# Optimization experiments

Hardware: AMD Instinct MI355X
Metric: run time of the kernel (lower is better)

## Reference

```python
import jax, jax.numpy as jnp
import numpy as np

D_MODEL = 512

def setup_inputs() -> dict:
    key = jax.random.key(0)
    k1, k2, k3 = jax.random.split(key, 3)
    B, N1, N2 = 16, 2048, 2048
    x1 = jax.random.normal(k1, (B, N1, D_MODEL), dtype=jnp.float32)
    x2 = jax.random.normal(k2, (B, N2, D_MODEL), dtype=jnp.float32)
    node_mask = jnp.ones((B, N1), dtype=jnp.bool_)
    # learned parameter: q_proj weight, stored torch-style [out, in]
    Wq = jax.random.normal(k3, (D_MODEL, D_MODEL), dtype=jnp.float32) * (1.0 / np.sqrt(D_MODEL))
    return {"x1": x1, "x2": x2, "node_mask": node_mask, "Wq": Wq}


def reference(x1, x2, node_mask, Wq):
    # Q = x1 @ Wq^T   (torch Linear with weight [out, in], no bias)
    Q = jnp.einsum('bnd,ed->bne', x1, Wq)            # [B, N1, 512]
    D = x2                                            # [B, N2, 512]
    # similarity matrix L = Q @ D^T
    L = jnp.einsum('bnd,bmd->bnm', Q, D)              # [B, N1, N2]
    # attention over document axis (dim=2)
    A_D = jax.nn.softmax(L, axis=2)                   # [B, N1, N2]
    # C_D = Q^T @ A_D -> transposed to [B, N2, 512]
    C_D = jnp.einsum('bnd,bnm->bmd', Q, A_D)          # [B, N2, 512]
    # attention over query axis (dim=1), then transposed: A_Q [B, N2, N1]
    A_Q = jnp.swapaxes(jax.nn.softmax(L, axis=1), 1, 2)
    # C_Q = D^T @ A_Q -> transposed to [B, N1, 512]
    C_Q = jnp.einsum('bmd,bmn->bnd', D, A_Q)          # [B, N1, 512]
    return (C_Q, C_D, A_D, A_Q)
```

## Files before the change

### kernel.cpp

```cpp
#include <hip/hip_runtime.h>

namespace {

constexpr int Bn = 16;
constexpr int Nn = 2048;
constexpr int Dn = 512;

typedef _Float16 h4 __attribute__((ext_vector_type(4)));
typedef _Float16 h8 __attribute__((ext_vector_type(8)));
typedef float    fx4 __attribute__((ext_vector_type(4)));

__device__ __forceinline__ void gld16(const _Float16* g, _Float16* l) {
  typedef const void __attribute__((address_space(1))) gvoid;
  typedef void __attribute__((address_space(3))) lvoid;
  __builtin_amdgcn_global_load_lds((gvoid*)g, (lvoid*)l, 16, 0, 0);
}

__device__ __forceinline__ void stage_gld(const _Float16* __restrict__ g, int ld,
    int r0, int k0, _Float16* __restrict__ lds, int t)
{
  #pragma unroll
  for (int i = 0; i < 2; ++i) {
    int chunk = i*256 + t;
    gld16(g + (long)(r0 + (chunk >> 2))*ld + k0 + (chunk & 3)*8, lds + chunk*8);
  }
}

__device__ __forceinline__ void stage_gld256(const _Float16* __restrict__ g, int ld,
    int r0, int k0, _Float16* __restrict__ lds, int t)
{
  #pragma unroll
  for (int i = 0; i < 4; ++i) {
    int chunk = i*256 + t;
    gld16(g + (long)(r0 + (chunk >> 2))*ld + k0 + (chunk & 3)*8, lds + chunk*8);
  }
}

__device__ __forceinline__ void load_f32(const float* __restrict__ g, int ld,
    int r0, int k0, int t, fx4* regs)
{
  #pragma unroll
  for (int rd = 0; rd < 4; ++rd)
    regs[rd] = *(const fx4*)(g + (long)(r0 + rd*32 + (t >> 3))*ld + k0 + (t & 7)*4);
}
template<int S>
__device__ __forceinline__ void write_cvt(const fx4* regs, _Float16* __restrict__ lds, int t)
{
  const int c = (t & 7)*4;
  #pragma unroll
  for (int rd = 0; rd < 4; ++rd) {
    int r = rd*32 + (t >> 3);
    h4 o;
    #pragma unroll
    for (int i = 0; i < 4; ++i) o[i] = (_Float16)regs[rd][i];
    *(h4*)(lds + r*S + c) = o;
  }
}

struct RegsA3 { h8 v0, v1; fx4 k00, k01, k10, k11; };
__device__ __forceinline__ void load_A3(const _Float16* __restrict__ g, int ld,
    int r0, int k0, int t, const float* __restrict__ kofs, RegsA3& R)
{
  {
    int chunk = t, r = chunk >> 2, c = (chunk & 3)*8;
    R.v0  = *(const h8*)(g + (long)(r0 + r)*ld + k0 + c);
    R.k00 = *(const fx4*)(kofs + k0 + c);
    R.k01 = *(const fx4*)(kofs + k0 + c + 4);
  }
  {
    int chunk = 256 + t, r = chunk >> 2, c = (chunk & 3)*8;
    R.v1  = *(const h8*)(g + (long)(r0 + r)*ld + k0 + c);
    R.k10 = *(const fx4*)(kofs + k0 + c);
    R.k11 = *(const fx4*)(kofs + k0 + c + 4);
  }
}
template<int S>
__device__ __forceinline__ void write_A3(const RegsA3& R, _Float16* __restrict__ lds, int t)
{
  {
    int chunk = t, r = chunk >> 2, c = (chunk & 3)*8;
    h8 o;
    #pragma unroll
    for (int j = 0; j < 4; ++j) {
      o[j]   = (_Float16)__expf((float)R.v0[j]   - R.k00[j]);
      o[4+j] = (_Float16)__expf((float)R.v0[4+j] - R.k01[j]);
    }
    *(h8*)(lds + r*S + c) = o;
  }
  {
    int chunk = 256 + t, r = chunk >> 2, c = (chunk & 3)*8;
    h8 o;
    #pragma unroll
    for (int j = 0; j < 4; ++j) {
      o[j]   = (_Float16)__expf((float)R.v1[j]   - R.k10[j]);
      o[4+j] = (_Float16)__expf((float)R.v1[4+j] - R.k11[j]);
    }
    *(h8*)(lds + r*S + c) = o;
  }
}

template<int MA, int MB, int EPI, int TY>
__global__ __launch_bounds__(256) void gemm128(
    const void* __restrict__ Ap, long sA,
    const void* __restrict__ Bp, long sB,
    void* __restrict__ Cp, long sC, int ldc,
    void* __restrict__ C2p, long sC2, int ldc2,
    int lda, int ldb, int K,
    const float* __restrict__ kofs,
    float* __restrict__ rowPM, float* __restrict__ rowPS,
    float* __restrict__ colPM, float* __restrict__ colPS)
{
  constexpr int SA = (MA == 0) ? 32 : 40;
  constexpr int SB = (MB == 0) ? 32 : 40;
  constexpr int ASZ = 128*SA, BSZ = 128*SB;
  constexpr int DB = 2*ASZ + 2*BSZ;
  constexpr int SMEM = (EPI >= 1 && DB < 128*136) ? 128*136 : DB;
  __shared__ _Float16 smem[SMEM];

  constexpr int TILES = 16*TY;
  const int bid = blockIdx.x;
  const int xcd = bid & 7, slot = bid >> 3;
  const int b = xcd*2 + slot/TILES;
  const int tile = slot % TILES;
  const int by = tile % TY, bx = tile / TY;
  const int row0 = bx*128, col0 = by*128;

  const int t = threadIdx.x, w = t >> 6, l = t & 63;
  const int wr = w >> 1, wc = w & 1, l15 = l & 15, lg = l >> 4;

  const void* Ab;
  const void* Bb;
  if constexpr (MA == 1) Ab = (const void*)((const float*)Ap + (long)b*sA);
  else                   Ab = (const void*)((const _Float16*)Ap + (long)b*sA);
  if constexpr (MB == 1) Bb = (const void*)((const float*)Bp + (long)b*sB);
  else                   Bb = (const void*)((const _Float16*)Bp + (long)b*sB);

  const float* ko = nullptr;
  if constexpr (MA == 3) ko = kofs + (long)b*Nn;

  fx4 acc[4][4];
  #pragma unroll
  for (int fi = 0; fi < 4; ++fi)
    #pragma unroll
    for (int fj = 0; fj < 4; ++fj)
      acc[fi][fj] = (fx4){0.f, 0.f, 0.f, 0.f};

  const int NT = K/32;
  fx4 regA[4], regB[4];
  RegsA3 rA3;

  if constexpr (MA == 0)      stage_gld((const _Float16*)Ab, lda, row0, 0, smem, t);
  else if constexpr (MA == 1) load_f32((const float*)Ab, lda, row0, 0, t, regA);
  else                        load_A3((const _Float16*)Ab, lda, row0, 0, t, ko, rA3);
  if constexpr (MB == 0)      stage_gld((const _Float16*)Bb, ldb, col0, 0, smem + 2*ASZ, t);
  else                        load_f32((const float*)Bb, ldb, col0, 0, t, regB);
  if constexpr (MA == 1)      write_cvt<SA>(regA, smem, t);
  if constexpr (MA == 3)      write_A3<SA>(rA3, smem, t);
  if constexpr (MB == 1)      write_cvt<SB>(regB, smem + 2*ASZ, t);
  __syncthreads();

  for (int kt = 0; kt < NT; ++kt) {
    const int cur = kt & 1, nxt = cur ^ 1;
    const int k1 = (kt + 1)*32;
    _Float16* cA = smem + cur*ASZ;
    _Float16* cB = smem + 2*ASZ + cur*BSZ;
    _Float16* nA = smem + nxt*ASZ;
    _Float16* nB = smem + 2*ASZ + nxt*BSZ;

    if (kt + 1 < NT) {
      if constexpr (MA == 0)      stage_gld((const _Float16*)Ab, lda, row0, k1, nA, t);
      else if constexpr (MA == 1) load_f32((const float*)Ab, lda, row0, k1, t, regA);
      else                        load_A3((const _Float16*)Ab, lda, row0, k1, t, ko, rA3);
      if constexpr (MB == 0)      stage_gld((const _Float16*)Bb, ldb, col0, k1, nB, t);
      else                        load_f32((const float*)Bb, ldb, col0, k1, t, regB);
    }

    h8 af[4], bf[4];
    #pragma unroll
    for (int fi = 0; fi < 4; ++fi)
      af[fi] = *(const h8*)(cA + (wr*64 + fi*16 + l15)*SA + lg*8);
    #pragma unroll
    for (int fj = 0; fj < 4; ++fj)
      bf[fj] = *(const h8*)(cB + (wc*64 + fj*16 + l15)*SB + lg*8);
    #pragma unroll
    for (int fi = 0; fi < 4; ++fi)
      #pragma unroll
      for (int fj = 0; fj < 4; ++fj)
        acc[fi][fj] = __builtin_amdgcn_mfma_f32_16x16x32_f16(af[fi], bf[fj], acc[fi][fj], 0, 0, 0);

    if (kt + 1 < NT) {
      if constexpr (MA == 1) write_cvt<SA>(regA, nA, t);
      if constexpr (MA == 3) write_A3<SA>(rA3, nA, t);
      if constexpr (MB == 1) write_cvt<SB>(regB, nB, t);
    }
    __syncthreads();
  }

  if constexpr (EPI == 0) {
    float* Cb = (float*)Cp + (long)b*sC;
    #pragma unroll
    for (int fi = 0; fi < 4; ++fi)
      #pragma unroll
      for (int fj = 0; fj < 4; ++fj)
        #pragma unroll
        for (int j = 0; j < 4; ++j)
          Cb[(long)(row0 + wr*64 + fi*16 + lg*4 + j)*ldc + col0 + wc*64 + fj*16 + l15] = acc[fi][fj][j];
  }

  if constexpr (EPI >= 1) {
    if constexpr (EPI == 1) {
      #pragma unroll
      for (int fi = 0; fi < 4; ++fi)
        #pragma unroll
        for (int fj = 0; fj < 4; ++fj)
          #pragma unroll
          for (int j = 0; j < 4; ++j)
            acc[fi][fj][j] = (float)(_Float16)acc[fi][fj][j];
    }

    #pragma unroll
    for (int fi = 0; fi < 4; ++fi) {
      #pragma unroll
      for (int j = 0; j < 4; ++j) {
        int rr = wr*64 + fi*16 + lg*4 + j;
        int key = (rr >> 3) & 7;
        #pragma unroll
        for (int fj = 0; fj < 4; ++fj) {
          int cc = wc*64 + fj*16 + l15;
          smem[rr*136 + ((((cc >> 3) ^ key) << 3) | (cc & 7))] = (_Float16)acc[fi][fj][j];
        }
      }
    }
    __syncthreads();
    _Float16* Cb  = (_Float16*)Cp  + (long)b*sC;
    _Float16* C2b = (_Float16*)C2p + (long)b*sC2;
    #pragma unroll
    for (int rd = 0; rd < 8; ++rd) {
      int r = rd*16 + (t >> 4);
      int g = (t & 15) ^ ((r >> 3) & 7);
      h8 v = *(const h8*)(smem + r*136 + g*8);
      *(h8*)(Cb + (long)(row0 + r)*ldc + col0 + (t & 15)*8) = v;
    }
    {
      const int q = t & 15, keyq = q & 7, n8 = q*8;
      #pragma unroll
      for (int rd = 0; rd < 8; ++rd) {
        int dl = rd*16 + (t >> 4);
        int gbase = ((dl >> 3) ^ keyq) << 3, c7 = dl & 7;
        h8 v;
        #pragma unroll
        for (int i = 0; i < 8; ++i)
          v[i] = smem[(n8 + i)*136 + gbase + c7];
        *(h8*)(C2b + (long)(col0 + dl)*ldc2 + row0 + n8) = v;
      }
    }
  }

  if constexpr (EPI == 1) {
    float rm[4][4], rs[4][4];
    #pragma unroll
    for (int fi = 0; fi < 4; ++fi)
      #pragma unroll
      for (int j = 0; j < 4; ++j)
        rm[fi][j] = fmaxf(fmaxf(acc[fi][0][j], acc[fi][1][j]),
                          fmaxf(acc[fi][2][j], acc[fi][3][j]));
    #pragma unroll
    for (int m = 1; m < 16; m <<= 1)
      #pragma unroll
      for (int fi = 0; fi < 4; ++fi)
        #pragma unroll
        for (int j = 0; j < 4; ++j)
          rm[fi][j] = fmaxf(rm[fi][j], __shfl_xor(rm[fi][j], m, 64));
    #pragma unroll
    for (int fi = 0; fi < 4; ++fi)
      #pragma unroll
      for (int j = 0; j < 4; ++j) {
        float s = 0.f;
        #pragma unroll
        for (int fj = 0; fj < 4; ++fj)
          s += __expf(acc[fi][fj][j] - rm[fi][j]);
        rs[fi][j] = s;
      }
    #pragma unroll
    for (int m = 1; m < 16; m <<= 1)
      #pragma unroll
      for (int fi = 0; fi < 4; ++fi)
        #pragma unroll
        for (int j = 0; j < 4; ++j)
          rs[fi][j] += __shfl_xor(rs[fi][j], m, 64);
    if (l15 == 0) {
      #pragma unroll
      for (int fi = 0; fi < 4; ++fi)
        #pragma unroll
        for (int j = 0; j < 4; ++j) {
          int row = row0 + wr*64 + fi*16 + lg*4 + j;
          long idx = ((long)b*Nn + row)*32 + by*2 + wc;
          rowPM[idx] = rm[fi][j];
          rowPS[idx] = rs[fi][j];
        }
    }
    float cm[4], cs[4];
    #pragma unroll
    for (int fj = 0; fj < 4; ++fj) {
      float v = -3.4e38f;
      #pragma unroll
      for (int fi = 0; fi < 4; ++fi)
        #pragma unroll
        for (int j = 0; j < 4; ++j)
          v = fmaxf(v, acc[fi][fj][j]);
      cm[fj] = v;
    }
    #pragma unroll
    for (int fj = 0; fj < 4; ++fj) {
      cm[fj] = fmaxf(cm[fj], __shfl_xor(cm[fj], 16, 64));
      cm[fj] = fmaxf(cm[fj], __shfl_xor(cm[fj], 32, 64));
    }
    #pragma unroll
    for (int fj = 0; fj < 4; ++fj) {
      float s = 0.f;
      #pragma unroll
      for (int fi = 0; fi < 4; ++fi)
        #pragma unroll
        for (int j = 0; j < 4; ++j)
          s += __expf(acc[fi][fj][j] - cm[fj]);
      cs[fj] = s;
    }
    #pragma unroll
    for (int fj = 0; fj < 4; ++fj) {
      cs[fj] += __shfl_xor(cs[fj], 16, 64);
      cs[fj] += __shfl_xor(cs[fj], 32, 64);
    }
    if (l < 16) {
      #pragma unroll
      for (int fj = 0; fj < 4; ++fj) {
        int col = col0 + wc*64 + fj*16 + l15;
        long idx = ((long)b*Nn + col)*32 + bx*2 + wr;
        colPM[idx] = cm[fj];
        colPS[idx] = cs[fj];
      }
    }
  }
}

__global__ __launch_bounds__(256, 2) void gemm_expw(
    const _Float16* __restrict__ Ap, const _Float16* __restrict__ Bp,
    float* __restrict__ Cp, const float* __restrict__ kofs)
{
  constexpr int SA = 40;
  constexpr int ASZ = 128*SA;
  constexpr int BSZ = 256*32;
  __shared__ _Float16 smem[2*ASZ + 2*BSZ];

  const int bid = blockIdx.x;
  const int xcd = bid & 7, slot = bid >> 3;
  const int b = xcd*2 + (slot >> 5);
  const int tile = slot & 31;
  const int by = tile & 1, bx = tile >> 1;
  const int row0 = bx*128, col0 = by*256;

  const int t = threadIdx.x, w = t >> 6, l = t & 63;
  const int wr = w >> 1, wc = w & 1, l15 = l & 15, lg = l >> 4;

  const _Float16* Ab = Ap + (long)b*Nn*Nn;
  const _Float16* Bb = Bp + (long)b*Dn*Nn;
  const float* ko = kofs + (long)b*Nn;

  fx4 acc[4][8];
  #pragma unroll
  for (int fi = 0; fi < 4; ++fi)
    #pragma unroll
    for (int fj = 0; fj < 8; ++fj)
      acc[fi][fj] = (fx4){0.f, 0.f, 0.f, 0.f};

  const int NT = Nn/32;
  RegsA3 rA3;

  load_A3(Ab, Nn, row0, 0, t, ko, rA3);
  stage_gld256(Bb, Nn, col0, 0, smem + 2*ASZ, t);
  write_A3<SA>(rA3, smem, t);
  __syncthreads();

  for (int kt = 0; kt < NT; ++kt) {
    const int cur = kt & 1, nxt = cur ^ 1;
    const int k1 = (kt + 1)*32;
    _Float16* cA = smem + cur*ASZ;
    _Float16* cB = smem + 2*ASZ + cur*BSZ;
    _Float16* nA = smem + nxt*ASZ;
    _Float16* nB = smem + 2*ASZ + nxt*BSZ;

    if (kt + 1 < NT) {
      load_A3(Ab, Nn, row0, k1, t, ko, rA3);
      stage_gld256(Bb, Nn, col0, k1, nB, t);
    }

    h8 af[4], bf[8];
    #pragma unroll
    for (int fi = 0; fi < 4; ++fi)
      af[fi] = *(const h8*)(cA + (wr*64 + fi*16 + l15)*SA + lg*8);
    #pragma unroll
    for (int fj = 0; fj < 8; ++fj)
      bf[fj] = *(const h8*)(cB + (wc*128 + fj*16 + l15)*32 + lg*8);
    #pragma unroll
    for (int fi = 0; fi < 4; ++fi)
      #pragma unroll
      for (int fj = 0; fj < 8; ++fj)
        acc[fi][fj] = __builtin_amdgcn_mfma_f32_16x16x32_f16(af[fi], bf[fj], acc[fi][fj], 0, 0, 0);

    if (kt + 1 < NT)
      write_A3<SA>(rA3, nA, t);
    __syncthreads();
  }

  float* Cb = Cp + (long)b*Nn*Dn;
  #pragma unroll
  for (int fi = 0; fi < 4; ++fi)
    #pragma unroll
    for (int fj = 0; fj < 8; ++fj)
      #pragma unroll
      for (int j = 0; j < 4; ++j)
        Cb[(long)(row0 + wr*64 + fi*16 + lg*4 + j)*Dn + col0 + wc*128 + fj*16 + l15] = acc[fi][fj][j];
}

__global__ __launch_bounds__(256) void convert_x2(const float* __restrict__ x2,
    _Float16* __restrict__ x2h, _Float16* __restrict__ x2hT)
{
  __shared__ _Float16 lt[64*66];
  const int b = blockIdx.z, m0 = blockIdx.x*64, d0 = blockIdx.y*64;
  const int t = threadIdx.x;
  const float* xb = x2 + (long)b*Nn*Dn;
  _Float16* hb = x2h + (long)b*Nn*Dn;
  #pragma unroll
  for (int rd = 0; rd < 4; ++rd) {
    int r = rd*16 + (t >> 4), c = (t & 15)*4;
    fx4 v = *(const fx4*)(xb + (long)(m0 + r)*Dn + d0 + c);
    h4 h;
    #pragma unroll
    for (int i = 0; i < 4; ++i) { h[i] = (_Float16)v[i]; lt[r*66 + c + i] = h[i]; }
    *(h4*)(hb + (long)(m0 + r)*Dn + d0 + c) = h;
  }
  __syncthreads();
  _Float16* tb = x2hT + (long)b*Dn*Nn;
  #pragma unroll
  for (int rd = 0; rd < 4; ++rd) {
    int dl = rd*16 + (t >> 4), ml = (t & 15)*4;
    h4 h;
    #pragma unroll
    for (int i = 0; i < 4; ++i) h[i] = lt[(ml + i)*66 + dl];
    *(h4*)(tb + (long)(d0 + dl)*Nn + m0 + ml) = h;
  }
}

__global__ __launch_bounds__(256) void reduce_stats(
    const float* __restrict__ rowPM, const float* __restrict__ rowPS,
    const float* __restrict__ colPM, const float* __restrict__ colPS,
    float* __restrict__ rofs, float* __restrict__ cofs)
{
  const int w = threadIdx.x >> 6, l = threadIdx.x & 63;
  const long row = (long)blockIdx.x*4 + w;
  const float* PM = blockIdx.y ? colPM : rowPM;
  const float* PS = blockIdx.y ? colPS : rowPS;
  float m0 = PM[row*32 + (l & 31)];
  float s0 = PS[row*32 + (l & 31)];
  float m = m0;
  #pragma unroll
  for (int k = 1; k < 32; k <<= 1) m = fmaxf(m, __shfl_xor(m, k, 64));
  float v = s0 * __expf(m0 - m);
  #pragma unroll
  for (int k = 1; k < 32; k <<= 1) v += __shfl_xor(v, k, 64);
  if (l == 0) {
    float ofs = m + __logf(v);
    if (blockIdx.y == 0) rofs[row] = ofs;
    else                 cofs[row] = ofs;
  }
}

__global__ __launch_bounds__(256) void finalize_AQ(const _Float16* __restrict__ Lh,
    float* __restrict__ AD, float* __restrict__ AQ,
    const float* __restrict__ rofs, const float* __restrict__ cofs)
{
  __shared__ float l2[64*65];
  const int b = blockIdx.z, n0 = blockIdx.x*64, m0 = blockIdx.y*64;
  const int t = threadIdx.x;
  const _Float16* Lb = Lh + (long)b*Nn*Nn;
  float* Db = AD + (long)b*Nn*Nn;
  #pragma unroll
  for (int rd = 0; rd < 4; ++rd) {
    int r = rd*16 + (t >> 4), c = (t & 15)*4;
    h4 v = *(const h4*)(Lb + (long)(n0 + r)*Nn + m0 + c);
    float ro = rofs[(long)b*Nn + n0 + r];
    fx4 co = *(const fx4*)(cofs + (long)b*Nn + m0 + c);
    fx4 e1;
    #pragma unroll
    for (int i = 0; i < 4; ++i) {
      float lv = (float)v[i];
      e1[i] = __expf(lv - ro);
      l2[r*65 + c + i] = __expf(lv - co[i]);
    }
    *(fx4*)(Db + (long)(n0 + r)*Nn + m0 + c) = e1;
  }
  __syncthreads();
  float* Qb = AQ + (long)b*Nn*Nn;
  #pragma unroll
  for (int rd = 0; rd < 4; ++rd) {
    int ml = rd*16 + (t >> 4), nl = (t & 15)*4;
    fx4 q;
    #pragma unroll
    for (int i = 0; i < 4; ++i) q[i] = l2[(nl + i)*65 + ml];
    *(fx4*)(Qb + (long)(m0 + ml)*Nn + n0 + nl) = q;
  }
}

}

extern "C" void kernel_launch(void* const* d_in, const int* in_sizes, int n_in,
                              void* d_out, int out_size, void* d_ws, size_t ws_size,
                              hipStream_t stream)
{
  const float* x1 = (const float*)d_in[0];
  const float* x2 = (const float*)d_in[1];
  const float* Wq = (const float*)d_in[3];

  float* out = (float*)d_out;
  float* C_Q = out;
  float* C_D = out + (long)Bn*Nn*Dn;
  float* A_D = out + 2L*Bn*Nn*Dn;
  float* A_Q = A_D + (long)Bn*Nn*Nn;

  char* ws = (char*)d_ws;
  _Float16* Qh   = (_Float16*)ws;
  _Float16* QhT  = Qh   + (long)Bn*Nn*Dn;
  _Float16* x2h  = QhT  + (long)Bn*Dn*Nn;
  _Float16* x2hT = x2h  + (long)Bn*Nn*Dn;
  _Float16* Lh   = x2hT + (long)Bn*Dn*Nn;
  float* rofs = (float*)(Lh + (long)Bn*Nn*Nn);
  float* cofs = rofs + (long)Bn*Nn;

  _Float16* Lt = (_Float16*)A_Q;
  float* rowPM = (float*)((char*)A_Q + sizeof(_Float16)*(long)Bn*Nn*Nn);
  float* rowPS = rowPM + (long)Bn*Nn*32;
  float* colPM = rowPS + (long)Bn*Nn*32;
  float* colPS = colPM + (long)Bn*Nn*32;

  dim3 blk(256);

  convert_x2<<<dim3(32, 8, 16), blk, 0, stream>>>(x2, x2h, x2hT);

  gemm128<1,1,2,4><<<dim3(1024), blk, 0, stream>>>(
      x1, (long)Nn*Dn, Wq, 0L,
      Qh, (long)Nn*Dn, Dn, QhT, (long)Dn*Nn, Nn,
      Dn, Dn, Dn,
      nullptr, nullptr, nullptr, nullptr, nullptr);

  gemm128<0,0,1,16><<<dim3(4096), blk, 0, stream>>>(
      Qh, (long)Nn*Dn, x2h, (long)Nn*Dn,
      Lh, (long)Nn*Nn, Nn, Lt, (long)Nn*Nn, Nn,
      Dn, Dn, Dn,
      nullptr, rowPM, rowPS, colPM, colPS);

  reduce_stats<<<dim3(Bn*Nn/4, 2), blk, 0, stream>>>(rowPM, rowPS, colPM, colPS, rofs, cofs);

  gemm_expw<<<dim3(512), blk, 0, stream>>>(Lh, x2hT, C_Q, cofs);

  gemm_expw<<<dim3(512), blk, 0, stream>>>(Lt, QhT, C_D, rofs);

  finalize_AQ<<<dim3(32, 32, 16), blk, 0, stream>>>(Lh, A_D, A_Q, rofs, cofs);
}
```

Before: 623.5 us.

## Fuse softmax output writes into exp-weighted GEMM kernels, drop finalize pass

Removes the separate finalize_AQ kernel and writes the A_Q and A_D softmax outputs directly from the gemm_expw kernels, reusing the fp16 L tiles they already load. Each of the two column blocks writes the alternating k-slices of its row tile. Lt scratch moves into the A_D buffer and the Lt-based GEMM runs first, so the scratch is consumed before A_D is overwritten. This removes one full re-read of the fp16 L matrix and the LDS transpose, but adds heavy fp32 global stores inside the GEMM loops and depends on the kernels running in that order.

Result: faster. 605.8 us (-2.8%).

```diff
diff --git a/kernel.cpp b/kernel.cpp
--- a/kernel.cpp
+++ b/kernel.cpp
@@ -97,6 +97,21 @@
     }
     *(h8*)(lds + r*S + c) = o;
   }
+}
+
+__device__ __forceinline__ void write_Of32(const RegsA3& R, float* __restrict__ base,
+    int ld, int r0, int k0, int t, float ro0, float ro1)
+{
+  const int r = t >> 2, c = (t & 3)*8;
+  float* d0 = base + (long)(r0 + r)*ld + k0 + c;
+  float* d1 = base + (long)(r0 + 64 + r)*ld + k0 + c;
+  fx4 a0, a1;
+  #pragma unroll
+  for (int j = 0; j < 4; ++j) { a0[j] = __expf((float)R.v0[j] - ro0); a1[j] = __expf((float)R.v0[4+j] - ro0); }
+  *(fx4*)d0 = a0; *(fx4*)(d0 + 4) = a1;
+  #pragma unroll
+  for (int j = 0; j < 4; ++j) { a0[j] = __expf((float)R.v1[j] - ro1); a1[j] = __expf((float)R.v1[4+j] - ro1); }
+  *(fx4*)d1 = a0; *(fx4*)(d1 + 4) = a1;
 }
 
 template<int MA, int MB, int EPI, int TY>
@@ -106,7 +121,6 @@
     void* __restrict__ Cp, long sC, int ldc,
     void* __restrict__ C2p, long sC2, int ldc2,
     int lda, int ldb, int K,
-    const float* __restrict__ kofs,
     float* __restrict__ rowPM, float* __restrict__ rowPS,
     float* __restrict__ colPM, float* __restrict__ colPS)
 {
@@ -135,9 +149,6 @@
   if constexpr (MB == 1) Bb = (const void*)((const float*)Bp + (long)b*sB);
   else                   Bb = (const void*)((const _Float16*)Bp + (long)b*sB);
 
-  const float* ko = nullptr;
-  if constexpr (MA == 3) ko = kofs + (long)b*Nn;
-
   fx4 acc[4][4];
   #pragma unroll
   for (int fi = 0; fi < 4; ++fi)
@@ -147,15 +158,12 @@
 
   const int NT = K/32;
   fx4 regA[4], regB[4];
-  RegsA3 rA3;
 
   if constexpr (MA == 0)      stage_gld((const _Float16*)Ab, lda, row0, 0, smem, t);
-  else if constexpr (MA == 1) load_f32((const float*)Ab, lda, row0, 0, t, regA);
-  else                        load_A3((const _Float16*)Ab, lda, row0, 0, t, ko, rA3);
+  else                        load_f32((const float*)Ab, lda, row0, 0, t, regA);
   if constexpr (MB == 0)      stage_gld((const _Float16*)Bb, ldb, col0, 0, smem + 2*ASZ, t);
   else                        load_f32((const float*)Bb, ldb, col0, 0, t, regB);
   if constexpr (MA == 1)      write_cvt<SA>(regA, smem, t);
-  if constexpr (MA == 3)      write_A3<SA>(rA3, smem, t);
   if constexpr (MB == 1)      write_cvt<SB>(regB, smem + 2*ASZ, t);
   __syncthreads();
 
@@ -169,8 +177,7 @@
 
     if (kt + 1 < NT) {
       if constexpr (MA == 0)      stage_gld((const _Float16*)Ab, lda, row0, k1, nA, t);
-      else if constexpr (MA == 1) load_f32((const float*)Ab, lda, row0, k1, t, regA);
-      else                        load_A3((const _Float16*)Ab, lda, row0, k1, t, ko, rA3);
+      else                        load_f32((const float*)Ab, lda, row0, k1, t, regA);
       if constexpr (MB == 0)      stage_gld((const _Float16*)Bb, ldb, col0, k1, nB, t);
       else                        load_f32((const float*)Bb, ldb, col0, k1, t, regB);
     }
@@ -190,21 +197,9 @@
 
     if (kt + 1 < NT) {
       if constexpr (MA == 1) write_cvt<SA>(regA, nA, t);
-      if constexpr (MA == 3) write_A3<SA>(rA3, nA, t);
       if constexpr (MB == 1) write_cvt<SB>(regB, nB, t);
     }
     __syncthreads();
-  }
-
-  if constexpr (EPI == 0) {
-    float* Cb = (float*)Cp + (long)b*sC;
-    #pragma unroll
-    for (int fi = 0; fi < 4; ++fi)
-      #pragma unroll
-      for (int fj = 0; fj < 4; ++fj)
-        #pragma unroll
-        for (int j = 0; j < 4; ++j)
-          Cb[(long)(row0 + wr*64 + fi*16 + lg*4 + j)*ldc + col0 + wc*64 + fj*16 + l15] = acc[fi][fj][j];
   }
 
   if constexpr (EPI >= 1) {
@@ -344,7 +339,8 @@
 
 __global__ __launch_bounds__(256, 2) void gemm_expw(
     const _Float16* __restrict__ Ap, const _Float16* __restrict__ Bp,
-    float* __restrict__ Cp, const float* __restrict__ kofs)
+    float* __restrict__ Cp, const float* __restrict__ kofs,
+    float* __restrict__ Ofull, const float* __restrict__ oofs)
 {
   constexpr int SA = 40;
   constexpr int ASZ = 128*SA;
@@ -364,6 +360,9 @@
   const _Float16* Ab = Ap + (long)b*Nn*Nn;
   const _Float16* Bb = Bp + (long)b*Dn*Nn;
   const float* ko = kofs + (long)b*Nn;
+  float* Ob = Ofull + (long)b*Nn*Nn;
+  const float ro0 = oofs[(long)b*Nn + row0 + (t >> 2)];
+  const float ro1 = oofs[(long)b*Nn + row0 + 64 + (t >> 2)];
 
   fx4 acc[4][8];
   #pragma unroll
@@ -378,6 +377,7 @@
   load_A3(Ab, Nn, row0, 0, t, ko, rA3);
   stage_gld256(Bb, Nn, col0, 0, smem + 2*ASZ, t);
   write_A3<SA>(rA3, smem, t);
+  if (by == 0) write_Of32(rA3, Ob, Nn, row0, 0, t, ro0, ro1);
   __syncthreads();
 
   for (int kt = 0; kt < NT; ++kt) {
@@ -406,8 +406,10 @@
       for (int fj = 0; fj < 8; ++fj)
         acc[fi][fj] = __builtin_amdgcn_mfma_f32_16x16x32_f16(af[fi], bf[fj], acc[fi][fj], 0, 0, 0);
 
-    if (kt + 1 < NT)
+    if (kt + 1 < NT) {
       write_A3<SA>(rA3, nA, t);
+      if (((kt + 1) & 1) == by) write_Of32(rA3, Ob, Nn, row0, k1, t, ro0, ro1);
+    }
     __syncthreads();
   }
 
@@ -471,42 +473,6 @@
     float ofs = m + __logf(v);
     if (blockIdx.y == 0) rofs[row] = ofs;
     else                 cofs[row] = ofs;
-  }
-}
-
-__global__ __launch_bounds__(256) void finalize_AQ(const _Float16* __restrict__ Lh,
-    float* __restrict__ AD, float* __restrict__ AQ,
-    const float* __restrict__ rofs, const float* __restrict__ cofs)
-{
-  __shared__ float l2[64*65];
-  const int b = blockIdx.z, n0 = blockIdx.x*64, m0 = blockIdx.y*64;
-  const int t = threadIdx.x;
-  const _Float16* Lb = Lh + (long)b*Nn*Nn;
-  float* Db = AD + (long)b*Nn*Nn;
-  #pragma unroll
-  for (int rd = 0; rd < 4; ++rd) {
-    int r = rd*16 + (t >> 4), c = (t & 15)*4;
-    h4 v = *(const h4*)(Lb + (long)(n0 + r)*Nn + m0 + c);
-    float ro = rofs[(long)b*Nn + n0 + r];
-    fx4 co = *(const fx4*)(cofs + (long)b*Nn + m0 + c);
-    fx4 e1;
-    #pragma unroll
-    for (int i = 0; i < 4; ++i) {
-      float lv = (float)v[i];
-      e1[i] = __expf(lv - ro);
-      l2[r*65 + c + i] = __expf(lv - co[i]);
-    }
-    *(fx4*)(Db + (long)(n0 + r)*Nn + m0 + c) = e1;
-  }
-  __syncthreads();
-  float* Qb = AQ + (long)b*Nn*Nn;
-  #pragma unroll
-  for (int rd = 0; rd < 4; ++rd) {
-    int ml = rd*16 + (t >> 4), nl = (t & 15)*4;
-    fx4 q;
-    #pragma unroll
-    for (int i = 0; i < 4; ++i) q[i] = l2[(nl + i)*65 + ml];
-    *(fx4*)(Qb + (long)(m0 + ml)*Nn + n0 + nl) = q;
   }
 }
 
@@ -535,8 +501,8 @@
   float* rofs = (float*)(Lh + (long)Bn*Nn*Nn);
   float* cofs = rofs + (long)Bn*Nn;
 
-  _Float16* Lt = (_Float16*)A_Q;
-  float* rowPM = (float*)((char*)A_Q + sizeof(_Float16)*(long)Bn*Nn*Nn);
+  _Float16* Lt = (_Float16*)A_D;
+  float* rowPM = (float*)((char*)A_D + sizeof(_Float16)*(long)Bn*Nn*Nn);
   float* rowPS = rowPM + (long)Bn*Nn*32;
   float* colPM = rowPS + (long)Bn*Nn*32;
   float* colPS = colPM + (long)Bn*Nn*32;
@@ -549,19 +515,17 @@
       x1, (long)Nn*Dn, Wq, 0L,
       Qh, (long)Nn*Dn, Dn, QhT, (long)Dn*Nn, Nn,
       Dn, Dn, Dn,
-      nullptr, nullptr, nullptr, nullptr, nullptr);
+      nullptr, nullptr, nullptr, nullptr);
 
   gemm128<0,0,1,16><<<dim3(4096), blk, 0, stream>>>(
       Qh, (long)Nn*Dn, x2h, (long)Nn*Dn,
       Lh, (long)Nn*Nn, Nn, Lt, (long)Nn*Nn, Nn,
       Dn, Dn, Dn,
-      nullptr, rowPM, rowPS, colPM, colPS);
+      rowPM, rowPS, colPM, colPS);
 
   reduce_stats<<<dim3(Bn*Nn/4, 2), blk, 0, stream>>>(rowPM, rowPS, colPM, colPS, rofs, cofs);
 
-  gemm_expw<<<dim3(512), blk, 0, stream>>>(Lh, x2hT, C_Q, cofs);
-
-  gemm_expw<<<dim3(512), blk, 0, stream>>>(Lt, QhT, C_D, rofs);
-
-  finalize_AQ<<<dim3(32, 32, 16), blk, 0, stream>>>(Lh, A_D, A_Q, rofs, cofs);
-}
+  gemm_expw<<<dim3(512), blk, 0, stream>>>(Lt, QhT, C_D, rofs, A_Q, cofs);
+
+  gemm_expw<<<dim3(512), blk, 0, stream>>>(Lh, x2hT, C_Q, cofs, A_D, rofs);
+}
```
